# Performance work log

Hardware: AMD Instinct MI355X
Metric: run time of the kernel (lower is better)

Reference implementation:

```python
import jax, jax.numpy as jnp
import numpy as np

T, B, D, H = 128, 32, 1024, 1024


def setup_inputs() -> dict:
    key = jax.random.key(0)
    k1, k2, k3 = jax.random.split(key, 3)
    s_in = 1.0 / np.sqrt(D)
    s_h = 1.0 / np.sqrt(H)
    x = jax.random.normal(k1, (T, B, D), dtype=jnp.float32)
    Wx = jax.random.normal(k2, (D, 4 * H), dtype=jnp.float32) * s_in
    Wh = jax.random.normal(k3, (H, 4 * H), dtype=jnp.float32) * s_h
    b = jnp.zeros((4 * H,), dtype=jnp.float32)
    return {"x": x, "Wx": Wx, "Wh": Wh, "b": b}


def reference(x, Wx, Wh, b):
    # RNN.forward with alpha=1 (scheduled-sampling branch dead) and future=0:
    # pure unroll of the LSTM cell over time dim 0, hidden starts at zero
    # (prev_hidden=None after reset()). hard=False -> sigmoid/tanh.
    Bsz = x.shape[1]
    h0 = jnp.zeros((Bsz, H), dtype=x.dtype)
    c0 = jnp.zeros((Bsz, H), dtype=x.dtype)

    def step(carry, xt):
        h, c = carry
        gates = xt @ Wx + h @ Wh + b  # [B, 4H]
        i, f, g, o = jnp.split(gates, 4, axis=-1)
        c_new = jax.nn.sigmoid(f) * c + jax.nn.sigmoid(i) * jnp.tanh(g)
        h_new = jax.nn.sigmoid(o) * jnp.tanh(c_new)
        return (h_new, c_new), h_new

    _, hs = jax.lax.scan(step, (h0, c0), x)  # hs: [T, B, H]
    return hs
```

## Files before the change

kernel.cpp:

```cpp
#include <hip/hip_runtime.h>
#include <hip/hip_bf16.h>
#include <stdint.h>

#define T_STEPS 128
#define BATCH   32
#define DIM     1024
#define HID     1024
#define NGATE   4096
#define MROWS   4096
#define NWGR    64

typedef unsigned int u32;
typedef __attribute__((ext_vector_type(8)))  __bf16 bf16x8;
typedef __attribute__((ext_vector_type(4)))  float  f32x4;
typedef __attribute__((ext_vector_type(16))) float  f32x16;
typedef __attribute__((ext_vector_type(4)))  u32    u32x4;

__device__ __forceinline__ unsigned short f2bf(float f) {
    u32 x = __float_as_uint(f);
    return (unsigned short)((x + 0x7fffu + ((x >> 16) & 1u)) >> 16);
}
__device__ __forceinline__ float sigf(float x) {
    return 1.0f / (1.0f + __expf(-x));
}
__device__ __forceinline__ float tanh_fast(float x) {
    float ax = fabsf(x);
    float e  = __expf(-2.0f * ax);
    float t  = (1.0f - e) / (1.0f + e);
    return copysignf(t, x);
}
__device__ __forceinline__ u32 umax2(u32 a, u32 b) { return a > b ? a : b; }

__device__ __forceinline__ void store_u32_coh(u32* p, u32 v) {
    asm volatile("global_store_dword %0, %1, off sc1" :: "v"(p), "v"(v) : "memory");
}


__global__ void fill_sentinel(u32* __restrict__ p, int n) {
    int i = (blockIdx.x * blockDim.x + threadIdx.x) * 4;
    if (i + 3 < n) {
        u32x4 v = {0xFFFFFFFFu, 0xFFFFFFFFu, 0xFFFFFFFFu, 0xFFFFFFFFu};
        *(u32x4*)(p + i) = v;
    }
}

__global__ void transpose_cast(const float* __restrict__ in,
                               unsigned short* __restrict__ out, int R, int C) {
    __shared__ float tile[32][33];
    int c0 = blockIdx.x * 32, r0 = blockIdx.y * 32;
    int tx = threadIdx.x, ty = threadIdx.y;
#pragma unroll
    for (int i = 0; i < 4; ++i)
        tile[ty + i * 8][tx] = in[(size_t)(r0 + ty + i * 8) * C + c0 + tx];
    __syncthreads();
#pragma unroll
    for (int i = 0; i < 4; ++i) {
        int cc = c0 + ty + i * 8;
        int rp = ((cc & 1023) << 2) | (cc >> 10);
        out[(size_t)rp * R + r0 + tx] = f2bf(tile[tx][ty + i * 8]);
    }
}

__global__ __launch_bounds__(256) void gemm_xw(
    const float* __restrict__ A,
    const unsigned short* __restrict__ BT,
    const float* __restrict__ bias,
    float* __restrict__ Gp) {
    __shared__ unsigned short As[128 * 32];
    __shared__ unsigned short Bs[128 * 32];
    int tid  = threadIdx.x;
    int wave = tid >> 6, lane = tid & 63;
    int q = lane >> 4, c = lane & 15;
    int wm = wave >> 1, wn = wave & 1;
    int tm = blockIdx.y * 128, tn = blockIdx.x * 128;

    f32x4 acc[4][4] = {};

    const int srow0 = tid >> 2;
    const int srow1 = 64 + (tid >> 2);
    const int scol  = (tid & 3) * 8;

    float4 a0l, a0h, a1l, a1h;
    u32x4 rb0, rb1;
    a0l = *(const float4*)(A + (size_t)(tm + srow0) * DIM + scol);
    a0h = *(const float4*)(A + (size_t)(tm + srow0) * DIM + scol + 4);
    a1l = *(const float4*)(A + (size_t)(tm + srow1) * DIM + scol);
    a1h = *(const float4*)(A + (size_t)(tm + srow1) * DIM + scol + 4);
    rb0 = *(const u32x4*)(BT + (size_t)(tn + srow0) * DIM + scol);
    rb1 = *(const u32x4*)(BT + (size_t)(tn + srow1) * DIM + scol);

    for (int kk = 0; kk < 32; ++kk) {
        __syncthreads();
        {
            u32x4 pa0 = { (u32)f2bf(a0l.x) | ((u32)f2bf(a0l.y) << 16),
                          (u32)f2bf(a0l.z) | ((u32)f2bf(a0l.w) << 16),
                          (u32)f2bf(a0h.x) | ((u32)f2bf(a0h.y) << 16),
                          (u32)f2bf(a0h.z) | ((u32)f2bf(a0h.w) << 16) };
            u32x4 pa1 = { (u32)f2bf(a1l.x) | ((u32)f2bf(a1l.y) << 16),
                          (u32)f2bf(a1l.z) | ((u32)f2bf(a1l.w) << 16),
                          (u32)f2bf(a1h.x) | ((u32)f2bf(a1h.y) << 16),
                          (u32)f2bf(a1h.z) | ((u32)f2bf(a1h.w) << 16) };
            *(u32x4*)(As + srow0 * 32 + scol) = pa0;
            *(u32x4*)(As + srow1 * 32 + scol) = pa1;
            *(u32x4*)(Bs + srow0 * 32 + scol) = rb0;
            *(u32x4*)(Bs + srow1 * 32 + scol) = rb1;
        }
        __syncthreads();
        if (kk < 31) {
            int ko = (kk + 1) * 32 + scol;
            a0l = *(const float4*)(A + (size_t)(tm + srow0) * DIM + ko);
            a0h = *(const float4*)(A + (size_t)(tm + srow0) * DIM + ko + 4);
            a1l = *(const float4*)(A + (size_t)(tm + srow1) * DIM + ko);
            a1h = *(const float4*)(A + (size_t)(tm + srow1) * DIM + ko + 4);
            rb0 = *(const u32x4*)(BT + (size_t)(tn + srow0) * DIM + ko);
            rb1 = *(const u32x4*)(BT + (size_t)(tn + srow1) * DIM + ko);
        }
        bf16x8 af[4], bfv[4];
#pragma unroll
        for (int i = 0; i < 4; ++i) {
            af[i]  = *(const bf16x8*)(As + (wm * 64 + i * 16 + c) * 32 + q * 8);
            bfv[i] = *(const bf16x8*)(Bs + (wn * 64 + i * 16 + c) * 32 + q * 8);
        }
#pragma unroll
        for (int i = 0; i < 4; ++i)
#pragma unroll
            for (int j = 0; j < 4; ++j)
                acc[i][j] = __builtin_amdgcn_mfma_f32_16x16x32_bf16(
                    af[i], bfv[j], acc[i][j], 0, 0, 0);
    }
#pragma unroll
    for (int j = 0; j < 4; ++j) {
        int co = tn + wn * 64 + j * 16 + c;
        float bj = bias[(co & 3) * 1024 + (co >> 2)];
        int wgr = co >> 6, cp = co & 63;
#pragma unroll
        for (int i = 0; i < 4; ++i) {
            int row0 = tm + wm * 64 + i * 16 + q * 4;
#pragma unroll
            for (int r = 0; r < 4; ++r)
                Gp[((size_t)wgr * MROWS + row0 + r) * 64 + cp] = acc[i][j][r] + bj;
        }
    }
}

__global__ __launch_bounds__(512, 1) void lstm_rec(
    const unsigned short* __restrict__ WhT,
    const float* __restrict__ Gp,
    unsigned short* hb,
    float* __restrict__ out) {
    __shared__ unsigned short Hs[32][1024];
    __shared__ float SlT[8][32][64];
    __shared__ unsigned short Ht[32][16];
    const int wg = blockIdx.x, tid = threadIdx.x;
    const int wv = tid >> 6, lane = tid & 63;
    const int ln = lane & 31, lh = lane >> 5;

    bf16x8 br0[8], br1[8];
    {
        const unsigned short* w0 =
            WhT + (size_t)(wg * 64 + ln) * DIM + wv * 128 + lh * 8;
        const unsigned short* w1 =
            WhT + (size_t)(wg * 64 + 32 + ln) * DIM + wv * 128 + lh * 8;
#pragma unroll
        for (int kk = 0; kk < 8; ++kk) {
            br0[kk] = *(const bf16x8*)(w0 + kk * 16);
            br1[kk] = *(const bf16x8*)(w1 + kk * 16);
        }
    }

    const int batch = tid >> 4, uu = tid & 15;
    float cs = 0.f;
    f32x4 ga = *(const f32x4*)(Gp + ((size_t)wg * MROWS + batch) * 64 + uu * 4);

    char* hs_base = (char*)&Hs[0][0];
    const int rxor = (ln & 15) << 4;

    for (int t = 0; t < T_STEPS; ++t) {
        if (t > 0) {
            const char* p0 = (const char*)hb + ((size_t)t << 16)
                           + ((size_t)wv << 13) + (size_t)lane * 16;
            const char* p1 = p0 + 4096;
            u32x4 h[8];
            for (;;) {
                asm volatile(
                    "global_load_dwordx4 %0, %8, off sc1\n\t"
                    "global_load_dwordx4 %1, %8, off offset:1024 sc1\n\t"
                    "global_load_dwordx4 %2, %8, off offset:2048 sc1\n\t"
                    "global_load_dwordx4 %3, %8, off offset:3072 sc1\n\t"
                    "global_load_dwordx4 %4, %9, off sc1\n\t"
                    "global_load_dwordx4 %5, %9, off offset:1024 sc1\n\t"
                    "global_load_dwordx4 %6, %9, off offset:2048 sc1\n\t"
                    "global_load_dwordx4 %7, %9, off offset:3072 sc1\n\t"
                    "s_waitcnt vmcnt(0)"
                    : "=&v"(h[0]), "=&v"(h[1]), "=&v"(h[2]), "=&v"(h[3]),
                      "=&v"(h[4]), "=&v"(h[5]), "=&v"(h[6]), "=&v"(h[7])
                    : "v"(p0), "v"(p1)
                    : "memory");
                u32 m = 0;
#pragma unroll
                for (int i = 0; i < 8; ++i) {
                    u32 a = umax2(umax2(h[i][0], h[i][1]),
                                  umax2(h[i][2], h[i][3]));
                    m = umax2(m, a);
                }
                if (!__any((int)(m == 0xFFFFFFFFu))) break;
            }
#pragma unroll
            for (int j = 0; j < 8; ++j) {
                int row  = (wv << 2) + (j >> 1);
                int colb = ((j & 1) << 10) + lane * 16;
                int off  = (row << 11) + (colb ^ ((row & 15) << 4));
                *(u32x4*)(hs_base + off) = h[j];
            }
            asm volatile("s_waitcnt lgkmcnt(0)" ::: "memory");
            __builtin_amdgcn_s_barrier();

            f32x16 acc0 = {}, acc1 = {};
            const char* hrow = hs_base + (ln << 11);
#pragma unroll
            for (int kk = 0; kk < 8; ++kk) {
                int cb = ((wv << 8) + (kk << 5) + (lh << 4)) ^ rxor;
                bf16x8 a = *(const bf16x8*)(hrow + cb);
                acc0 = __builtin_amdgcn_mfma_f32_32x32x16_bf16(a, br0[kk], acc0, 0, 0, 0);
                acc1 = __builtin_amdgcn_mfma_f32_32x32x16_bf16(a, br1[kk], acc1, 0, 0, 0);
            }

#pragma unroll
            for (int rg = 0; rg < 4; ++rg)
#pragma unroll
                for (int rr = 0; rr < 4; ++rr) {
                    const int bb = rg * 8 + lh * 4 + rr;
                    SlT[wv][bb][ln]      = acc0[rg * 4 + rr];
                    SlT[wv][bb][32 + ln] = acc1[rg * 4 + rr];
                }
            asm volatile("s_waitcnt lgkmcnt(0)" ::: "memory");
            __builtin_amdgcn_s_barrier();
        }

        f32x4 gv = ga;
        if (t > 0) {
#pragma unroll
            for (int ks = 0; ks < 8; ++ks)
                gv += *(const f32x4*)&SlT[ks][batch][uu * 4];
        }
        float cn = sigf(gv[1]) * cs + sigf(gv[0]) * tanh_fast(gv[2]);
        cs = cn;
        float hv = sigf(gv[3]) * tanh_fast(cn);

        Ht[batch][uu] = f2bf(hv);
        asm volatile("s_waitcnt lgkmcnt(0)" ::: "memory");
        if ((uu & 1) == 0) {
            u32 packed = *(const u32*)&Ht[batch][uu];
            store_u32_coh((u32*)(hb + (size_t)(t + 1) * (BATCH * HID)
                                    + (size_t)batch * HID + wg * 16 + uu), packed);
        }

        if (t + 1 < T_STEPS)
            ga = *(const f32x4*)(Gp + ((size_t)wg * MROWS + (size_t)(t + 1) * 32 + batch) * 64
                                 + uu * 4);
        out[((size_t)t * BATCH + batch) * HID + wg * 16 + uu] = hv;
    }
}


extern "C" void kernel_launch(void* const* d_in, const int* in_sizes, int n_in,
                              void* d_out, int out_size, void* d_ws, size_t ws_size,
                              hipStream_t stream) {
    const float* x  = (const float*)d_in[0];
    const float* Wx = (const float*)d_in[1];
    const float* Wh = (const float*)d_in[2];
    const float* b  = (const float*)d_in[3];
    float* out = (float*)d_out;

    char* ws = (char*)d_ws;
    const size_t OFF_WXT  = 8ull  << 20;
    const size_t OFF_WHT  = 16ull << 20;
    const size_t OFF_G    = 24ull << 20;
    const size_t OFF_HB   = 88ull << 20;
    const size_t NEEDED   = OFF_HB + (size_t)(T_STEPS + 1) * BATCH * HID * 2;
    if (ws_size < NEEDED) return;

    unsigned short* WxT = (unsigned short*)(ws + OFF_WXT);
    unsigned short* WhT = (unsigned short*)(ws + OFF_WHT);
    float*          Gp  = (float*)(ws + OFF_G);
    unsigned short* hb  = (unsigned short*)(ws + OFF_HB);

    const int HBW = (T_STEPS + 1) * BATCH * HID / 2;
    fill_sentinel<<<(HBW / 4 + 255) / 256, 256, 0, stream>>>((u32*)hb, HBW);
    dim3 tb(32, 8);
    transpose_cast<<<dim3(NGATE / 32, DIM / 32), tb, 0, stream>>>(Wx, WxT, DIM, NGATE);
    transpose_cast<<<dim3(NGATE / 32, HID / 32), tb, 0, stream>>>(Wh, WhT, HID, NGATE);

    gemm_xw<<<dim3(NGATE / 128, MROWS / 128), 256, 0, stream>>>(x, WxT, b, Gp);

    lstm_rec<<<NWGR, 512, 0, stream>>>(WhT, Gp, hb, out);
}
```

Measured before the change: 480.1 us.

## Fuse input-projection GEMM into recurrent kernel with sentinel-polled overlap

Merges the x·Wx GEMM and the LSTM recurrence into one launch. Extra GEMM blocks sit after the 64 recurrent workgroups and write gate pre-activations with coherent stores. Recurrent blocks poll those values against a sentinel, so early timesteps can start while later GEMM tiles are still running. The cost is a second 64MB sentinel fill of the gate buffer, a large shared-memory footprint that limits the GEMM blocks to one per CU, and a dependence on the recurrent blocks being resident first.

```diff
diff --git a/kernel.cpp b/kernel.cpp
--- a/kernel.cpp
+++ b/kernel.cpp
@@ -9,6 +9,7 @@
 #define NGATE   4096
 #define MROWS   4096
 #define NWGR    64
+#define NGEMM   1024
 
 typedef unsigned int u32;
 typedef __attribute__((ext_vector_type(8)))  __bf16 bf16x8;
@@ -34,6 +35,9 @@
 __device__ __forceinline__ void store_u32_coh(u32* p, u32 v) {
     asm volatile("global_store_dword %0, %1, off sc1" :: "v"(p), "v"(v) : "memory");
 }
+__device__ __forceinline__ void store_f32_coh(float* p, float v) {
+    asm volatile("global_store_dword %0, %1, off sc1" :: "v"(p), "v"(v) : "memory");
+}
 
 
 __global__ void fill_sentinel(u32* __restrict__ p, int n) {
@@ -61,98 +65,89 @@
     }
 }
 
-__global__ __launch_bounds__(256) void gemm_xw(
-    const float* __restrict__ A,
-    const unsigned short* __restrict__ BT,
+__global__ __launch_bounds__(512, 1) void lstm_fused(
+    const float* __restrict__ x,
+    const unsigned short* __restrict__ WxT,
+    const unsigned short* __restrict__ WhT,
     const float* __restrict__ bias,
-    float* __restrict__ Gp) {
-    __shared__ unsigned short As[128 * 32];
-    __shared__ unsigned short Bs[128 * 32];
-    int tid  = threadIdx.x;
-    int wave = tid >> 6, lane = tid & 63;
-    int q = lane >> 4, c = lane & 15;
-    int wm = wave >> 1, wn = wave & 1;
-    int tm = blockIdx.y * 128, tn = blockIdx.x * 128;
-
-    f32x4 acc[4][4] = {};
-
-    const int srow0 = tid >> 2;
-    const int srow1 = 64 + (tid >> 2);
-    const int scol  = (tid & 3) * 8;
-
-    float4 a0l, a0h, a1l, a1h;
-    u32x4 rb0, rb1;
-    a0l = *(const float4*)(A + (size_t)(tm + srow0) * DIM + scol);
-    a0h = *(const float4*)(A + (size_t)(tm + srow0) * DIM + scol + 4);
-    a1l = *(const float4*)(A + (size_t)(tm + srow1) * DIM + scol);
-    a1h = *(const float4*)(A + (size_t)(tm + srow1) * DIM + scol + 4);
-    rb0 = *(const u32x4*)(BT + (size_t)(tn + srow0) * DIM + scol);
-    rb1 = *(const u32x4*)(BT + (size_t)(tn + srow1) * DIM + scol);
-
-    for (int kk = 0; kk < 32; ++kk) {
-        __syncthreads();
-        {
-            u32x4 pa0 = { (u32)f2bf(a0l.x) | ((u32)f2bf(a0l.y) << 16),
-                          (u32)f2bf(a0l.z) | ((u32)f2bf(a0l.w) << 16),
-                          (u32)f2bf(a0h.x) | ((u32)f2bf(a0h.y) << 16),
-                          (u32)f2bf(a0h.z) | ((u32)f2bf(a0h.w) << 16) };
-            u32x4 pa1 = { (u32)f2bf(a1l.x) | ((u32)f2bf(a1l.y) << 16),
-                          (u32)f2bf(a1l.z) | ((u32)f2bf(a1l.w) << 16),
-                          (u32)f2bf(a1h.x) | ((u32)f2bf(a1h.y) << 16),
-                          (u32)f2bf(a1h.z) | ((u32)f2bf(a1h.w) << 16) };
-            *(u32x4*)(As + srow0 * 32 + scol) = pa0;
-            *(u32x4*)(As + srow1 * 32 + scol) = pa1;
-            *(u32x4*)(Bs + srow0 * 32 + scol) = rb0;
-            *(u32x4*)(Bs + srow1 * 32 + scol) = rb1;
-        }
-        __syncthreads();
-        if (kk < 31) {
-            int ko = (kk + 1) * 32 + scol;
-            a0l = *(const float4*)(A + (size_t)(tm + srow0) * DIM + ko);
-            a0h = *(const float4*)(A + (size_t)(tm + srow0) * DIM + ko + 4);
-            a1l = *(const float4*)(A + (size_t)(tm + srow1) * DIM + ko);
-            a1h = *(const float4*)(A + (size_t)(tm + srow1) * DIM + ko + 4);
-            rb0 = *(const u32x4*)(BT + (size_t)(tn + srow0) * DIM + ko);
-            rb1 = *(const u32x4*)(BT + (size_t)(tn + srow1) * DIM + ko);
-        }
-        bf16x8 af[4], bfv[4];
-#pragma unroll
-        for (int i = 0; i < 4; ++i) {
-            af[i]  = *(const bf16x8*)(As + (wm * 64 + i * 16 + c) * 32 + q * 8);
-            bfv[i] = *(const bf16x8*)(Bs + (wn * 64 + i * 16 + c) * 32 + q * 8);
-        }
-#pragma unroll
-        for (int i = 0; i < 4; ++i)
-#pragma unroll
-            for (int j = 0; j < 4; ++j)
-                acc[i][j] = __builtin_amdgcn_mfma_f32_16x16x32_bf16(
-                    af[i], bfv[j], acc[i][j], 0, 0, 0);
-    }
-#pragma unroll
-    for (int j = 0; j < 4; ++j) {
-        int co = tn + wn * 64 + j * 16 + c;
-        float bj = bias[(co & 3) * 1024 + (co >> 2)];
-        int wgr = co >> 6, cp = co & 63;
-#pragma unroll
-        for (int i = 0; i < 4; ++i) {
-            int row0 = tm + wm * 64 + i * 16 + q * 4;
-#pragma unroll
-            for (int r = 0; r < 4; ++r)
-                Gp[((size_t)wgr * MROWS + row0 + r) * 64 + cp] = acc[i][j][r] + bj;
-        }
-    }
-}
-
-__global__ __launch_bounds__(512, 1) void lstm_rec(
-    const unsigned short* __restrict__ WhT,
-    const float* __restrict__ Gp,
+    float* __restrict__ Gp,
     unsigned short* hb,
     float* __restrict__ out) {
     __shared__ unsigned short Hs[32][1024];
     __shared__ float SlT[8][32][64];
     __shared__ unsigned short Ht[32][16];
-    const int wg = blockIdx.x, tid = threadIdx.x;
-    const int wv = tid >> 6, lane = tid & 63;
+    __shared__ unsigned short As[128 * 32];
+    __shared__ unsigned short Bs[128 * 32];
+
+    const int tid = threadIdx.x;
+    const int wave = tid >> 6, lane = tid & 63;
+
+    if (blockIdx.x >= NWGR) {
+        const int g  = blockIdx.x - NWGR;
+        const int bx = g & 31, by = g >> 5;
+        const int tm = by * 128, tn = bx * 128;
+        const int q = lane >> 4, c = lane & 15;
+        const int wm = wave >> 2, wn = wave & 3;
+
+        f32x4 acc[4][2] = {};
+        const int srow = tid >> 2;
+        const int scol = (tid & 3) * 8;
+
+        float4 a0l, a0h; u32x4 rb0;
+        a0l = *(const float4*)(x + (size_t)(tm + srow) * DIM + scol);
+        a0h = *(const float4*)(x + (size_t)(tm + srow) * DIM + scol + 4);
+        rb0 = *(const u32x4*)(WxT + (size_t)(tn + srow) * DIM + scol);
+
+        for (int kk = 0; kk < 32; ++kk) {
+            __syncthreads();
+            {
+                u32x4 pa = { (u32)f2bf(a0l.x) | ((u32)f2bf(a0l.y) << 16),
+                             (u32)f2bf(a0l.z) | ((u32)f2bf(a0l.w) << 16),
+                             (u32)f2bf(a0h.x) | ((u32)f2bf(a0h.y) << 16),
+                             (u32)f2bf(a0h.z) | ((u32)f2bf(a0h.w) << 16) };
+                *(u32x4*)(As + srow * 32 + scol) = pa;
+                *(u32x4*)(Bs + srow * 32 + scol) = rb0;
+            }
+            __syncthreads();
+            if (kk < 31) {
+                int ko = (kk + 1) * 32 + scol;
+                a0l = *(const float4*)(x + (size_t)(tm + srow) * DIM + ko);
+                a0h = *(const float4*)(x + (size_t)(tm + srow) * DIM + ko + 4);
+                rb0 = *(const u32x4*)(WxT + (size_t)(tn + srow) * DIM + ko);
+            }
+            bf16x8 af[4], bfv[2];
+#pragma unroll
+            for (int i = 0; i < 4; ++i)
+                af[i] = *(const bf16x8*)(As + (wm * 64 + i * 16 + c) * 32 + q * 8);
+#pragma unroll
+            for (int j = 0; j < 2; ++j)
+                bfv[j] = *(const bf16x8*)(Bs + (wn * 32 + j * 16 + c) * 32 + q * 8);
+#pragma unroll
+            for (int i = 0; i < 4; ++i)
+#pragma unroll
+                for (int j = 0; j < 2; ++j)
+                    acc[i][j] = __builtin_amdgcn_mfma_f32_16x16x32_bf16(
+                        af[i], bfv[j], acc[i][j], 0, 0, 0);
+        }
+#pragma unroll
+        for (int j = 0; j < 2; ++j) {
+            int co = tn + wn * 32 + j * 16 + c;
+            float bj = bias[(co & 3) * 1024 + (co >> 2)];
+            int wgr = co >> 6, cp = co & 63;
+#pragma unroll
+            for (int i = 0; i < 4; ++i) {
+                int row0 = tm + wm * 64 + i * 16 + q * 4;
+#pragma unroll
+                for (int r = 0; r < 4; ++r)
+                    store_f32_coh(&Gp[((size_t)wgr * MROWS + row0 + r) * 64 + cp],
+                                  acc[i][j][r] + bj);
+            }
+        }
+        return;
+    }
+
+    const int wg = blockIdx.x;
+    const int wv = wave;
     const int ln = lane & 31, lh = lane >> 5;
 
     bf16x8 br0[8], br1[8];
@@ -170,7 +165,17 @@
 
     const int batch = tid >> 4, uu = tid & 15;
     float cs = 0.f;
-    f32x4 ga = *(const f32x4*)(Gp + ((size_t)wg * MROWS + batch) * 64 + uu * 4);
+
+    u32x4 gau;
+    {
+        const float* p = Gp + ((size_t)wg * MROWS + batch) * 64 + uu * 4;
+        for (;;) {
+            asm volatile("global_load_dwordx4 %0, %1, off sc1\n\ts_waitcnt vmcnt(0)"
+                         : "=&v"(gau) : "v"(p) : "memory");
+            u32 m = umax2(umax2(gau[0], gau[1]), umax2(gau[2], gau[3]));
+            if (!__any((int)(m == 0xFFFFFFFFu))) break;
+        }
+    }
 
     char* hs_base = (char*)&Hs[0][0];
     const int rxor = (ln & 15) << 4;
@@ -237,7 +242,19 @@
             __builtin_amdgcn_s_barrier();
         }
 
-        f32x4 gv = ga;
+        {
+            u32 m = umax2(umax2(gau[0], gau[1]), umax2(gau[2], gau[3]));
+            if (__any((int)(m == 0xFFFFFFFFu))) {
+                const float* p = Gp + ((size_t)wg * MROWS + (size_t)t * 32 + batch) * 64
+                               + uu * 4;
+                do {
+                    asm volatile("global_load_dwordx4 %0, %1, off sc1\n\ts_waitcnt vmcnt(0)"
+                                 : "=&v"(gau) : "v"(p) : "memory");
+                    m = umax2(umax2(gau[0], gau[1]), umax2(gau[2], gau[3]));
+                } while (__any((int)(m == 0xFFFFFFFFu)));
+            }
+        }
+        f32x4 gv = __builtin_bit_cast(f32x4, gau);
         if (t > 0) {
 #pragma unroll
             for (int ks = 0; ks < 8; ++ks)
@@ -255,9 +272,12 @@
                                     + (size_t)batch * HID + wg * 16 + uu), packed);
         }
 
-        if (t + 1 < T_STEPS)
-            ga = *(const f32x4*)(Gp + ((size_t)wg * MROWS + (size_t)(t + 1) * 32 + batch) * 64
-                                 + uu * 4);
+        if (t + 1 < T_STEPS) {
+            const float* p = Gp + ((size_t)wg * MROWS + (size_t)(t + 1) * 32 + batch) * 64
+                           + uu * 4;
+            asm volatile("global_load_dwordx4 %0, %1, off sc1"
+                         : "=&v"(gau) : "v"(p) : "memory");
+        }
         out[((size_t)t * BATCH + batch) * HID + wg * 16 + uu] = hv;
     }
 }
@@ -287,11 +307,11 @@
 
     const int HBW = (T_STEPS + 1) * BATCH * HID / 2;
     fill_sentinel<<<(HBW / 4 + 255) / 256, 256, 0, stream>>>((u32*)hb, HBW);
+    const int GPW = NWGR * MROWS * 64;
+    fill_sentinel<<<(GPW / 4 + 255) / 256, 256, 0, stream>>>((u32*)Gp, GPW);
     dim3 tb(32, 8);
     transpose_cast<<<dim3(NGATE / 32, DIM / 32), tb, 0, stream>>>(Wx, WxT, DIM, NGATE);
     transpose_cast<<<dim3(NGATE / 32, HID / 32), tb, 0, stream>>>(Wh, WhT, HID, NGATE);
 
-    gemm_xw<<<dim3(NGATE / 128, MROWS / 128), 256, 0, stream>>>(x, WxT, b, Gp);
-
-    lstm_rec<<<NWGR, 512, 0, stream>>>(WhT, Gp, hb, out);
-}
+    lstm_fused<<<NWGR + NGEMM, 512, 0, stream>>>(x, WxT, WhT, b, Gp, hb, out);
+}
```

After: 657.1 us. +36.9%, slower.
